# Kernel optimization log

Measured on AMD Instinct MI355X. Metric: run time of the kernel, lower is better.

The kernel has to match this reference:

```python
import jax, jax.numpy as jnp
import numpy as np

N = {"drug": 20000, "gene": 80000, "disease": 20000}
E = 800000
D = 128  # in_size = hidden_size = out_size
ETYPES = [("drug", "treats", "disease"), ("drug", "targets", "gene"),
          ("gene", "assoc", "disease"), ("disease", "rev_treats", "drug")]


def setup_inputs() -> dict:
    key = jax.random.key(0)
    ks = iter(jax.random.split(key, 64))
    inp = {}
    for nt in ["drug", "gene", "disease"]:
        inp[f"feat_{nt}"] = jax.random.normal(next(ks), (N[nt], D), jnp.float32)
    for layer in (1, 2):
        for (_, e, _) in ETYPES:
            inp[f"W{layer}_{e}"] = jax.random.normal(next(ks), (D, D), jnp.float32) / np.sqrt(D).astype(np.float32)
            inp[f"b{layer}_{e}"] = jnp.zeros((D,), jnp.float32)
    for (s, e, d) in ETYPES:
        inp[f"src_{e}"] = jax.random.randint(next(ks), (E,), 0, N[s], jnp.int32)
        inp[f"dst_{e}"] = jax.random.randint(next(ks), (E,), 0, N[d], jnp.int32)
        inp[f"neg_dst_{e}"] = jax.random.randint(next(ks), (E,), 0, N[d], jnp.int32)
    return inp


def _rgcn_layer(feats, W, b, src, dst):
    # per-etype Linear -> copy_u -> per-dst mean, summed across etypes ('sum' cross reducer)
    out = {nt: jnp.zeros((N[nt], D), jnp.float32) for nt in N}
    for (s, e, d) in ETYPES:
        Wh = feats[s] @ W[e] + b[e]                          # [N_s, D]
        msg = Wh[src[e]]                                     # [E, D] gather
        ssum = jax.ops.segment_sum(msg, dst[e], num_segments=N[d])
        cnt = jax.ops.segment_sum(jnp.ones((E,), jnp.float32), dst[e], num_segments=N[d])
        out[d] = out[d] + ssum / jnp.maximum(cnt, 1.0)[:, None]
    return out


def _dot_scores(h, src, dst):
    # DotProductPredictor: sigmoid(u . v) per edge, concatenated over etypes
    return jnp.concatenate([
        jax.nn.sigmoid(jnp.sum(h[s][src[e]] * h[d][dst[e]], axis=-1))
        for (s, e, d) in ETYPES])


def reference(feat_drug, feat_gene, feat_disease,
              W1_treats, b1_treats, W1_targets, b1_targets, W1_assoc, b1_assoc,
              W1_rev_treats, b1_rev_treats,
              W2_treats, b2_treats, W2_targets, b2_targets, W2_assoc, b2_assoc,
              W2_rev_treats, b2_rev_treats,
              src_treats, dst_treats, src_targets, dst_targets,
              src_assoc, dst_assoc, src_rev_treats, dst_rev_treats,
              neg_dst_treats, neg_dst_targets, neg_dst_assoc, neg_dst_rev_treats):
    feats = {"drug": feat_drug, "gene": feat_gene, "disease": feat_disease}
    W1 = {"treats": W1_treats, "targets": W1_targets, "assoc": W1_assoc, "rev_treats": W1_rev_treats}
    b1 = {"treats": b1_treats, "targets": b1_targets, "assoc": b1_assoc, "rev_treats": b1_rev_treats}
    W2 = {"treats": W2_treats, "targets": W2_targets, "assoc": W2_assoc, "rev_treats": W2_rev_treats}
    b2 = {"treats": b2_treats, "targets": b2_targets, "assoc": b2_assoc, "rev_treats": b2_rev_treats}
    src = {"treats": src_treats, "targets": src_targets, "assoc": src_assoc, "rev_treats": src_rev_treats}
    dst = {"treats": dst_treats, "targets": dst_targets, "assoc": dst_assoc, "rev_treats": dst_rev_treats}
    neg_dst = {"treats": neg_dst_treats, "targets": neg_dst_targets,
               "assoc": neg_dst_assoc, "rev_treats": neg_dst_rev_treats}

    h1 = _rgcn_layer(feats, W1, b1, src, dst)
    h1 = {k: jax.nn.leaky_relu(v, 0.01) for k, v in h1.items()}  # F.leaky_relu default slope
    h2 = _rgcn_layer(h1, W2, b2, src, dst)
    out_pos = _dot_scores(h2, src, dst)       # positive graph = G's own edges
    out_neg = _dot_scores(h2, src, neg_dst)   # negative graph: corrupted dst
    return jnp.concatenate([out_pos, out_neg])  # [2 * 4 * E]
```

## Files before the change

kernel.cpp:

```cpp
#include <hip/hip_runtime.h>
#include <hip/hip_bf16.h>
#include <cstddef>

#define NE 800000
#define NCNT 140000
#define NBLK 137

typedef unsigned short ushortT;

__device__ __forceinline__ float lrelu01(float x) { return x > 0.f ? x : 0.01f * x; }
__device__ __forceinline__ float blo(int v) { return __uint_as_float(((unsigned)v) << 16); }
__device__ __forceinline__ float bhi(int v) { return __uint_as_float(((unsigned)v) & 0xffff0000u); }
__device__ __forceinline__ ushortT f2b(float x) {
  unsigned u = __float_as_uint(x);
  unsigned r = (u + 0x7fffu + ((u >> 16) & 1u)) >> 16;
  return (ushortT)r;
}

__global__ __launch_bounds__(256) void count_kernel(const int* d0, const int* d1,
                                                    const int* d2, const int* d3,
                                                    int* __restrict__ cnt) {
  const int e = blockIdx.y;
  const int* dst = e == 0 ? d0 : e == 1 ? d1 : e == 2 ? d2 : d3;
  int* c = cnt + (e == 0 ? 0 : e == 1 ? 20000 : e == 2 ? 100000 : 120000);
  int stride = gridDim.x * blockDim.x;
  for (int i = blockIdx.x * blockDim.x + threadIdx.x; i < NE; i += stride)
    atomicAdd(&c[dst[i]], 1);
}

__global__ __launch_bounds__(256) void inv_kernel(const int* __restrict__ cnt,
                                                  float* __restrict__ inv, int n) {
  int i = blockIdx.x * blockDim.x + threadIdx.x;
  if (i < n) {
    int c = cnt[i];
    inv[i] = 1.0f / (float)(c > 1 ? c : 1);
  }
}

__global__ __launch_bounds__(256) void psum_kernel(const int* __restrict__ cnt,
                                                   int* __restrict__ bsum, int n) {
  __shared__ int red[4];
  const int tid = threadIdx.x;
  const int base = blockIdx.x * 1024;
  int s = 0;
#pragma unroll
  for (int k = 0; k < 4; ++k) {
    int i = base + tid + 256 * k;
    s += (i < n) ? cnt[i] : 0;
  }
#pragma unroll
  for (int off = 32; off >= 1; off >>= 1) s += __shfl_xor(s, off, 64);
  if ((tid & 63) == 0) red[tid >> 6] = s;
  __syncthreads();
  if (tid == 0) bsum[blockIdx.x] = red[0] + red[1] + red[2] + red[3];
}

__global__ __launch_bounds__(256) void bscan_kernel(const int* __restrict__ bsum,
                                                    int* __restrict__ bex,
                                                    int* __restrict__ gscan, int nb, int n) {
  __shared__ int sh[256];
  const int tid = threadIdx.x;
  sh[tid] = (tid < nb) ? bsum[tid] : 0;
  __syncthreads();
  for (int off = 1; off < 256; off <<= 1) {
    int add = (tid >= off) ? sh[tid - off] : 0;
    __syncthreads();
    sh[tid] += add;
    __syncthreads();
  }
  if (tid < nb) bex[tid] = (tid == 0) ? 0 : sh[tid - 1];
  if (tid == nb - 1) gscan[n] = sh[tid];
}

__global__ __launch_bounds__(256) void scanout_kernel(const int* __restrict__ cnt,
                                                      const int* __restrict__ bex,
                                                      int* __restrict__ gscan, int n) {
  __shared__ int part[256];
  const int tid = threadIdx.x;
  const int base = blockIdx.x * 1024 + tid * 4;
  int v0 = (base + 0 < n) ? cnt[base + 0] : 0;
  int v1 = (base + 1 < n) ? cnt[base + 1] : 0;
  int v2 = (base + 2 < n) ? cnt[base + 2] : 0;
  int v3 = (base + 3 < n) ? cnt[base + 3] : 0;
  part[tid] = v0 + v1 + v2 + v3;
  __syncthreads();
  for (int off = 1; off < 256; off <<= 1) {
    int add = (tid >= off) ? part[tid - off] : 0;
    __syncthreads();
    part[tid] += add;
    __syncthreads();
  }
  int ex = bex[blockIdx.x] + ((tid == 0) ? 0 : part[tid - 1]);
  if (base + 0 < n) gscan[base + 0] = ex;
  ex += v0;
  if (base + 1 < n) gscan[base + 1] = ex;
  ex += v1;
  if (base + 2 < n) gscan[base + 2] = ex;
  ex += v2;
  if (base + 3 < n) gscan[base + 3] = ex;
}

__global__ __launch_bounds__(256) void place_kernel(const int* s0, const int* s1,
                                                    const int* s2, const int* s3,
                                                    const int* d0, const int* d1,
                                                    const int* d2, const int* d3,
                                                    const int* __restrict__ gscan,
                                                    int* __restrict__ cursor,
                                                    int* __restrict__ csr) {
  const int e = blockIdx.y;
  const int* src = e == 0 ? s0 : e == 1 ? s1 : e == 2 ? s2 : s3;
  const int* dst = e == 0 ? d0 : e == 1 ? d1 : e == 2 ? d2 : d3;
  const int co = e == 0 ? 0 : e == 1 ? 20000 : e == 2 ? 100000 : 120000;
  const int wr = e == 0 ? 0 : e == 1 ? 20000 : e == 2 ? 40000 : 120000;
  int stride = gridDim.x * blockDim.x;
  for (int i = blockIdx.x * blockDim.x + threadIdx.x; i < NE; i += stride) {
    int d = dst[i];
    int p = gscan[co + d] + atomicAdd(&cursor[co + d], 1);
    csr[p] = src[i] + wr;
  }
}

template <bool LRELU>
__global__ __launch_bounds__(256) void gemm_kernel(const float* X0, const float* X1,
                                                   const float* X2, const float* X3,
                                                   const float* W0, const float* W1,
                                                   const float* W2, const float* W3,
                                                   const float* B0, const float* B1,
                                                   const float* B2, const float* B3,
                                                   ushortT* __restrict__ out) {
  __shared__ float Ws[128 * 128];
  __shared__ float xs[32 * 128];
  const int tid = threadIdx.x;
  const int bid = blockIdx.x;

  int lrow0, wo;
  const float *X, *W, *B;
  if (bid < 625)       { lrow0 = bid * 32;          X = X0; W = W0; B = B0; wo = 0; }
  else if (bid < 1250) { lrow0 = (bid - 625) * 32;  X = X1; W = W1; B = B1; wo = 20000; }
  else if (bid < 3750) { lrow0 = (bid - 1250) * 32; X = X2; W = W2; B = B2; wo = 40000; }
  else                 { lrow0 = (bid - 3750) * 32; X = X3; W = W3; B = B3; wo = 120000; }

  {
    const float4* Wv = (const float4*)W;
    float4* Wsv = (float4*)Ws;
#pragma unroll
    for (int i = 0; i < 16; ++i) Wsv[tid + 256 * i] = Wv[tid + 256 * i];
  }
  {
    float4* xsv = (float4*)xs;
#pragma unroll
    for (int i = 0; i < 4; ++i) {
      int f = tid + 256 * i;
      int rr = f >> 5;
      int c4 = f & 31;
      float4 v = *(const float4*)(X + (size_t)(lrow0 + rr) * 128 + c4 * 4);
      if (LRELU) {
        v.x = lrelu01(v.x); v.y = lrelu01(v.y); v.z = lrelu01(v.z); v.w = lrelu01(v.w);
      }
      xsv[f] = v;
    }
  }
  __syncthreads();

  const int c = tid & 31;
  const int r = tid >> 5;
  const float4 bv = *(const float4*)(B + c * 4);
  float acc[4][4];
#pragma unroll
  for (int ri = 0; ri < 4; ++ri) {
    acc[ri][0] = bv.x; acc[ri][1] = bv.y; acc[ri][2] = bv.z; acc[ri][3] = bv.w;
  }

#pragma unroll 8
  for (int k0 = 0; k0 < 128; k0 += 4) {
    const float4 w0 = *(const float4*)(Ws + (k0 + 0) * 128 + c * 4);
    const float4 w1 = *(const float4*)(Ws + (k0 + 1) * 128 + c * 4);
    const float4 w2 = *(const float4*)(Ws + (k0 + 2) * 128 + c * 4);
    const float4 w3 = *(const float4*)(Ws + (k0 + 3) * 128 + c * 4);
#pragma unroll
    for (int ri = 0; ri < 4; ++ri) {
      const float4 xv = *(const float4*)(xs + (r + 8 * ri) * 128 + k0);
      acc[ri][0] = fmaf(xv.x, w0.x, acc[ri][0]);
      acc[ri][0] = fmaf(xv.y, w1.x, acc[ri][0]);
      acc[ri][0] = fmaf(xv.z, w2.x, acc[ri][0]);
      acc[ri][0] = fmaf(xv.w, w3.x, acc[ri][0]);
      acc[ri][1] = fmaf(xv.x, w0.y, acc[ri][1]);
      acc[ri][1] = fmaf(xv.y, w1.y, acc[ri][1]);
      acc[ri][1] = fmaf(xv.z, w2.y, acc[ri][1]);
      acc[ri][1] = fmaf(xv.w, w3.y, acc[ri][1]);
      acc[ri][2] = fmaf(xv.x, w0.z, acc[ri][2]);
      acc[ri][2] = fmaf(xv.y, w1.z, acc[ri][2]);
      acc[ri][2] = fmaf(xv.z, w2.z, acc[ri][2]);
      acc[ri][2] = fmaf(xv.w, w3.z, acc[ri][2]);
      acc[ri][3] = fmaf(xv.x, w0.w, acc[ri][3]);
      acc[ri][3] = fmaf(xv.y, w1.w, acc[ri][3]);
      acc[ri][3] = fmaf(xv.z, w2.w, acc[ri][3]);
      acc[ri][3] = fmaf(xv.w, w3.w, acc[ri][3]);
    }
  }

#pragma unroll
  for (int ri = 0; ri < 4; ++ri) {
    int gr = wo + lrow0 + r + 8 * ri;
    ushort4 o;
    o.x = f2b(acc[ri][0]); o.y = f2b(acc[ri][1]);
    o.z = f2b(acc[ri][2]); o.w = f2b(acc[ri][3]);
    *(ushort4*)(out + (size_t)gr * 128 + c * 4) = o;
  }
}

template <bool OUT_BF16, int NSLOT>
__global__ __launch_bounds__(256) void gather_kernel(const ushortT* __restrict__ Wh,
                                                     const int* __restrict__ csr,
                                                     const int* __restrict__ gscan,
                                                     const float* __restrict__ inv,
                                                     int slot0, int slot1,
                                                     void* __restrict__ outv, int nnode) {
  const int lane = threadIdx.x & 63;
  const int q = lane >> 4;
  const int ql = lane & 15;
  int w = (blockIdx.x * blockDim.x + threadIdx.x) >> 6;
  const int nw = (gridDim.x * blockDim.x) >> 6;
  for (int d = w; d < nnode; d += nw) {
    float a0 = 0.f, a1 = 0.f, a2 = 0.f, a3 = 0.f, a4 = 0.f, a5 = 0.f, a6 = 0.f, a7 = 0.f;
#pragma unroll
    for (int k = 0; k < NSLOT; ++k) {
      const int slot = (k == 0 ? slot0 : slot1) + d;
      const int beg = gscan[slot];
      const int end = gscan[slot + 1];
      float t0 = 0.f, t1 = 0.f, t2 = 0.f, t3 = 0.f, t4 = 0.f, t5 = 0.f, t6 = 0.f, t7 = 0.f;
      for (int c0 = beg; c0 < end; c0 += 64) {
        int m = end - c0;
        if (m > 64) m = 64;
        int idx = (c0 + lane < end) ? csr[c0 + lane] : 0;
        for (int j = 0; j < m; j += 4) {
          int jj = j + q;
          int s = __shfl(idx, jj < m ? jj : 0, 64);
          if (jj < m) {
            const int4 v = *(const int4*)(Wh + (size_t)s * 128 + ql * 8);
            t0 += blo(v.x); t1 += bhi(v.x);
            t2 += blo(v.y); t3 += bhi(v.y);
            t4 += blo(v.z); t5 += bhi(v.z);
            t6 += blo(v.w); t7 += bhi(v.w);
          }
        }
      }
      const float ic = inv[slot];
      a0 = fmaf(t0, ic, a0); a1 = fmaf(t1, ic, a1);
      a2 = fmaf(t2, ic, a2); a3 = fmaf(t3, ic, a3);
      a4 = fmaf(t4, ic, a4); a5 = fmaf(t5, ic, a5);
      a6 = fmaf(t6, ic, a6); a7 = fmaf(t7, ic, a7);
    }
    a0 += __shfl_xor(a0, 16, 64); a0 += __shfl_xor(a0, 32, 64);
    a1 += __shfl_xor(a1, 16, 64); a1 += __shfl_xor(a1, 32, 64);
    a2 += __shfl_xor(a2, 16, 64); a2 += __shfl_xor(a2, 32, 64);
    a3 += __shfl_xor(a3, 16, 64); a3 += __shfl_xor(a3, 32, 64);
    a4 += __shfl_xor(a4, 16, 64); a4 += __shfl_xor(a4, 32, 64);
    a5 += __shfl_xor(a5, 16, 64); a5 += __shfl_xor(a5, 32, 64);
    a6 += __shfl_xor(a6, 16, 64); a6 += __shfl_xor(a6, 32, 64);
    a7 += __shfl_xor(a7, 16, 64); a7 += __shfl_xor(a7, 32, 64);
    if (lane < 16) {
      if (OUT_BF16) {
        ushortT* out = (ushortT*)outv;
        int4 o;
        o.x = (int)f2b(a0) | ((int)f2b(a1) << 16);
        o.y = (int)f2b(a2) | ((int)f2b(a3) << 16);
        o.z = (int)f2b(a4) | ((int)f2b(a5) << 16);
        o.w = (int)f2b(a6) | ((int)f2b(a7) << 16);
        *(int4*)(out + (size_t)d * 128 + ql * 8) = o;
      } else {
        float* out = (float*)outv;
        *(float4*)(out + (size_t)d * 128 + ql * 8) = make_float4(a0, a1, a2, a3);
        *(float4*)(out + (size_t)d * 128 + ql * 8 + 4) = make_float4(a4, a5, a6, a7);
      }
    }
  }
}

__global__ __launch_bounds__(256) void score_kernel(const ushortT* __restrict__ hs,
                                                    const ushortT* __restrict__ hd,
                                                    const int* __restrict__ src,
                                                    const int* __restrict__ dst,
                                                    const int* __restrict__ ndst,
                                                    float* __restrict__ outp,
                                                    float* __restrict__ outn) {
  const int lane = threadIdx.x & 63;
  const int q = lane >> 4;
  const int ql = lane & 15;
  int w = (blockIdx.x * blockDim.x + threadIdx.x) >> 6;
  const int nw = (gridDim.x * blockDim.x) >> 6;
  for (int base = 4 * w; base < NE; base += 4 * nw) {
    int e = base + q;
    int s = src[e], d = dst[e], n = ndst[e];
    const int4 av = *(const int4*)(hs + (size_t)s * 128 + ql * 8);
    const int4 bv = *(const int4*)(hd + (size_t)d * 128 + ql * 8);
    const int4 cv = *(const int4*)(hd + (size_t)n * 128 + ql * 8);
    float dp = blo(av.x) * blo(bv.x) + bhi(av.x) * bhi(bv.x)
             + blo(av.y) * blo(bv.y) + bhi(av.y) * bhi(bv.y)
             + blo(av.z) * blo(bv.z) + bhi(av.z) * bhi(bv.z)
             + blo(av.w) * blo(bv.w) + bhi(av.w) * bhi(bv.w);
    float dn = blo(av.x) * blo(cv.x) + bhi(av.x) * bhi(cv.x)
             + blo(av.y) * blo(cv.y) + bhi(av.y) * bhi(cv.y)
             + blo(av.z) * blo(cv.z) + bhi(av.z) * bhi(cv.z)
             + blo(av.w) * blo(cv.w) + bhi(av.w) * bhi(cv.w);
#pragma unroll
    for (int off = 1; off <= 8; off <<= 1) {
      dp += __shfl_xor(dp, off, 64);
      dn += __shfl_xor(dn, off, 64);
    }
    if (ql == 0) {
      outp[e] = 1.0f / (1.0f + expf(-dp));
      outn[e] = 1.0f / (1.0f + expf(-dn));
    }
  }
}

extern "C" void kernel_launch(void* const* d_in, const int* in_sizes, int n_in,
                              void* d_out, int out_size, void* d_ws, size_t ws_size,
                              hipStream_t stream) {
  const float* feat[3] = {(const float*)d_in[0], (const float*)d_in[1], (const float*)d_in[2]};
  const float *W1[4], *b1[4], *W2[4], *b2[4];
  for (int e = 0; e < 4; ++e) {
    W1[e] = (const float*)d_in[3 + 2 * e];
    b1[e] = (const float*)d_in[4 + 2 * e];
    W2[e] = (const float*)d_in[11 + 2 * e];
    b2[e] = (const float*)d_in[12 + 2 * e];
  }
  const int *src[4], *dst[4], *ndst[4];
  for (int e = 0; e < 4; ++e) {
    src[e] = (const int*)d_in[19 + 3 * e];
    dst[e] = (const int*)d_in[20 + 3 * e];
    ndst[e] = (const int*)d_in[21 + 3 * e];
  }

  ushortT* WhAll = (ushortT*)d_ws;
  float* h1 = (float*)(WhAll + (size_t)140000 * 128);
  ushortT* h2 = (ushortT*)(h1 + (size_t)120000 * 128);
  int* cnt = (int*)(h2 + (size_t)120000 * 128);
  float* inv = (float*)(cnt + NCNT);
  int* gscan = (int*)(inv + NCNT);
  int* cursor = gscan + NCNT + 1;
  int* bsum = cursor + NCNT;
  int* bex = bsum + 256;
  int* csr = bex + 256;

  hipMemsetAsync(cnt, 0, NCNT * 4, stream);
  hipMemsetAsync(cursor, 0, NCNT * 4, stream);

  const size_t HD = 0, HG = 20000, HS = 100000;

  count_kernel<<<dim3(512, 4), 256, 0, stream>>>(dst[0], dst[1], dst[2], dst[3], cnt);
  inv_kernel<<<(NCNT + 255) / 256, 256, 0, stream>>>(cnt, inv, NCNT);
  psum_kernel<<<NBLK, 256, 0, stream>>>(cnt, bsum, NCNT);
  bscan_kernel<<<1, 256, 0, stream>>>(bsum, bex, gscan, NBLK, NCNT);
  scanout_kernel<<<NBLK, 256, 0, stream>>>(cnt, bex, gscan, NCNT);
  place_kernel<<<dim3(512, 4), 256, 0, stream>>>(src[0], src[1], src[2], src[3],
                                                 dst[0], dst[1], dst[2], dst[3],
                                                 gscan, cursor, csr);

  gemm_kernel<false><<<4375, 256, 0, stream>>>(
      feat[0], feat[0], feat[1], feat[2],
      W1[0], W1[1], W1[2], W1[3], b1[0], b1[1], b1[2], b1[3], WhAll);
  gather_kernel<false, 1><<<2048, 256, 0, stream>>>(WhAll, csr, gscan, inv, 120000, 0,
                                                    (void*)(h1 + HD * 128), 20000);
  gather_kernel<false, 1><<<2048, 256, 0, stream>>>(WhAll, csr, gscan, inv, 20000, 0,
                                                    (void*)(h1 + HG * 128), 80000);
  gather_kernel<false, 2><<<2048, 256, 0, stream>>>(WhAll, csr, gscan, inv, 0, 100000,
                                                    (void*)(h1 + HS * 128), 20000);

  gemm_kernel<true><<<4375, 256, 0, stream>>>(
      h1 + HD * 128, h1 + HD * 128, h1 + HG * 128, h1 + HS * 128,
      W2[0], W2[1], W2[2], W2[3], b2[0], b2[1], b2[2], b2[3], WhAll);
  gather_kernel<true, 1><<<2048, 256, 0, stream>>>(WhAll, csr, gscan, inv, 120000, 0,
                                                   (void*)(h2 + HD * 128), 20000);
  gather_kernel<true, 1><<<2048, 256, 0, stream>>>(WhAll, csr, gscan, inv, 20000, 0,
                                                   (void*)(h2 + HG * 128), 80000);
  gather_kernel<true, 2><<<2048, 256, 0, stream>>>(WhAll, csr, gscan, inv, 0, 100000,
                                                   (void*)(h2 + HS * 128), 20000);

  const size_t sh[4] = {HD, HD, HG, HS};
  const size_t dh[4] = {HS, HG, HS, HD};
  float* out = (float*)d_out;
  for (int e = 0; e < 4; ++e) {
    score_kernel<<<2048, 256, 0, stream>>>(h2 + sh[e] * 128, h2 + dh[e] * 128,
                                           src[e], dst[e], ndst[e], out + (size_t)e * NE,
                                           out + (size_t)(4 + e) * NE);
  }
}
```

Baseline: 1.095 ms.

## Remap gather to quarter-wave per node, store h1 as bf16, fuse preprocessing kernels

The gather kernel now assigns one 16-lane group to each destination node instead of a full wavefront, removing the cross-group shuffle reduction and issuing four row loads per step. Layer-1 hidden features are stored as bf16, and the second GEMM reads bf16 input, which halves that traffic but adds rounding. The inverse-count computation and cursor initialisation move into the scan kernel, so one launch and one memset go away. The score kernel processes two edges per group per iteration to raise memory-level parallelism.

Result: no change. 1.092 ms (-0.2%).

```diff
diff --git a/kernel.cpp b/kernel.cpp
--- a/kernel.cpp
+++ b/kernel.cpp
@@ -26,15 +26,6 @@
   int stride = gridDim.x * blockDim.x;
   for (int i = blockIdx.x * blockDim.x + threadIdx.x; i < NE; i += stride)
     atomicAdd(&c[dst[i]], 1);
-}
-
-__global__ __launch_bounds__(256) void inv_kernel(const int* __restrict__ cnt,
-                                                  float* __restrict__ inv, int n) {
-  int i = blockIdx.x * blockDim.x + threadIdx.x;
-  if (i < n) {
-    int c = cnt[i];
-    inv[i] = 1.0f / (float)(c > 1 ? c : 1);
-  }
 }
 
 __global__ __launch_bounds__(256) void psum_kernel(const int* __restrict__ cnt,
@@ -74,7 +65,9 @@
 
 __global__ __launch_bounds__(256) void scanout_kernel(const int* __restrict__ cnt,
                                                       const int* __restrict__ bex,
-                                                      int* __restrict__ gscan, int n) {
+                                                      int* __restrict__ gscan,
+                                                      int* __restrict__ cursor,
+                                                      float* __restrict__ inv, int n) {
   __shared__ int part[256];
   const int tid = threadIdx.x;
   const int base = blockIdx.x * 1024 + tid * 4;
@@ -91,20 +84,19 @@
     __syncthreads();
   }
   int ex = bex[blockIdx.x] + ((tid == 0) ? 0 : part[tid - 1]);
-  if (base + 0 < n) gscan[base + 0] = ex;
+  if (base + 0 < n) { gscan[base+0] = ex; cursor[base+0] = ex; inv[base+0] = 1.0f/(float)(v0>1?v0:1); }
   ex += v0;
-  if (base + 1 < n) gscan[base + 1] = ex;
+  if (base + 1 < n) { gscan[base+1] = ex; cursor[base+1] = ex; inv[base+1] = 1.0f/(float)(v1>1?v1:1); }
   ex += v1;
-  if (base + 2 < n) gscan[base + 2] = ex;
+  if (base + 2 < n) { gscan[base+2] = ex; cursor[base+2] = ex; inv[base+2] = 1.0f/(float)(v2>1?v2:1); }
   ex += v2;
-  if (base + 3 < n) gscan[base + 3] = ex;
+  if (base + 3 < n) { gscan[base+3] = ex; cursor[base+3] = ex; inv[base+3] = 1.0f/(float)(v3>1?v3:1); }
 }
 
 __global__ __launch_bounds__(256) void place_kernel(const int* s0, const int* s1,
                                                     const int* s2, const int* s3,
                                                     const int* d0, const int* d1,
                                                     const int* d2, const int* d3,
-                                                    const int* __restrict__ gscan,
                                                     int* __restrict__ cursor,
                                                     int* __restrict__ csr) {
   const int e = blockIdx.y;
@@ -114,15 +106,14 @@
   const int wr = e == 0 ? 0 : e == 1 ? 20000 : e == 2 ? 40000 : 120000;
   int stride = gridDim.x * blockDim.x;
   for (int i = blockIdx.x * blockDim.x + threadIdx.x; i < NE; i += stride) {
-    int d = dst[i];
-    int p = gscan[co + d] + atomicAdd(&cursor[co + d], 1);
+    int p = atomicAdd(&cursor[co + dst[i]], 1);
     csr[p] = src[i] + wr;
   }
 }
 
-template <bool LRELU>
-__global__ __launch_bounds__(256) void gemm_kernel(const float* X0, const float* X1,
-                                                   const float* X2, const float* X3,
+template <bool LRELU, bool XBF16>
+__global__ __launch_bounds__(256) void gemm_kernel(const void* X0v, const void* X1v,
+                                                   const void* X2v, const void* X3v,
                                                    const float* W0, const float* W1,
                                                    const float* W2, const float* W3,
                                                    const float* B0, const float* B1,
@@ -134,11 +125,12 @@
   const int bid = blockIdx.x;
 
   int lrow0, wo;
-  const float *X, *W, *B;
-  if (bid < 625)       { lrow0 = bid * 32;          X = X0; W = W0; B = B0; wo = 0; }
-  else if (bid < 1250) { lrow0 = (bid - 625) * 32;  X = X1; W = W1; B = B1; wo = 20000; }
-  else if (bid < 3750) { lrow0 = (bid - 1250) * 32; X = X2; W = W2; B = B2; wo = 40000; }
-  else                 { lrow0 = (bid - 3750) * 32; X = X3; W = W3; B = B3; wo = 120000; }
+  const void* Xv;
+  const float *W, *B;
+  if (bid < 625)       { lrow0 = bid * 32;          Xv = X0v; W = W0; B = B0; wo = 0; }
+  else if (bid < 1250) { lrow0 = (bid - 625) * 32;  Xv = X1v; W = W1; B = B1; wo = 20000; }
+  else if (bid < 3750) { lrow0 = (bid - 1250) * 32; Xv = X2v; W = W2; B = B2; wo = 40000; }
+  else                 { lrow0 = (bid - 3750) * 32; Xv = X3v; W = W3; B = B3; wo = 120000; }
 
   {
     const float4* Wv = (const float4*)W;
@@ -146,7 +138,26 @@
 #pragma unroll
     for (int i = 0; i < 16; ++i) Wsv[tid + 256 * i] = Wv[tid + 256 * i];
   }
-  {
+  if (XBF16) {
+    const ushortT* X = (const ushortT*)Xv;
+#pragma unroll
+    for (int i = 0; i < 2; ++i) {
+      int f = tid + 256 * i;
+      int rr = f >> 4;
+      int c8 = f & 15;
+      int4 v = *(const int4*)(X + (size_t)(lrow0 + rr) * 128 + c8 * 8);
+      float x0 = blo(v.x), x1 = bhi(v.x), x2 = blo(v.y), x3 = bhi(v.y);
+      float x4 = blo(v.z), x5 = bhi(v.z), x6 = blo(v.w), x7 = bhi(v.w);
+      if (LRELU) {
+        x0 = lrelu01(x0); x1 = lrelu01(x1); x2 = lrelu01(x2); x3 = lrelu01(x3);
+        x4 = lrelu01(x4); x5 = lrelu01(x5); x6 = lrelu01(x6); x7 = lrelu01(x7);
+      }
+      float* p = xs + rr * 128 + c8 * 8;
+      *(float4*)(p) = make_float4(x0, x1, x2, x3);
+      *(float4*)(p + 4) = make_float4(x4, x5, x6, x7);
+    }
+  } else {
+    const float* X = (const float*)Xv;
     float4* xsv = (float4*)xs;
 #pragma unroll
     for (int i = 0; i < 4; ++i) {
@@ -209,72 +220,63 @@
   }
 }
 
-template <bool OUT_BF16, int NSLOT>
+template <int NSLOT>
 __global__ __launch_bounds__(256) void gather_kernel(const ushortT* __restrict__ Wh,
                                                      const int* __restrict__ csr,
                                                      const int* __restrict__ gscan,
                                                      const float* __restrict__ inv,
                                                      int slot0, int slot1,
-                                                     void* __restrict__ outv, int nnode) {
+                                                     ushortT* __restrict__ out, int nnode) {
   const int lane = threadIdx.x & 63;
-  const int q = lane >> 4;
   const int ql = lane & 15;
-  int w = (blockIdx.x * blockDim.x + threadIdx.x) >> 6;
-  const int nw = (gridDim.x * blockDim.x) >> 6;
-  for (int d = w; d < nnode; d += nw) {
-    float a0 = 0.f, a1 = 0.f, a2 = 0.f, a3 = 0.f, a4 = 0.f, a5 = 0.f, a6 = 0.f, a7 = 0.f;
-#pragma unroll
-    for (int k = 0; k < NSLOT; ++k) {
-      const int slot = (k == 0 ? slot0 : slot1) + d;
-      const int beg = gscan[slot];
-      const int end = gscan[slot + 1];
-      float t0 = 0.f, t1 = 0.f, t2 = 0.f, t3 = 0.f, t4 = 0.f, t5 = 0.f, t6 = 0.f, t7 = 0.f;
-      for (int c0 = beg; c0 < end; c0 += 64) {
-        int m = end - c0;
-        if (m > 64) m = 64;
-        int idx = (c0 + lane < end) ? csr[c0 + lane] : 0;
-        for (int j = 0; j < m; j += 4) {
-          int jj = j + q;
-          int s = __shfl(idx, jj < m ? jj : 0, 64);
-          if (jj < m) {
-            const int4 v = *(const int4*)(Wh + (size_t)s * 128 + ql * 8);
-            t0 += blo(v.x); t1 += bhi(v.x);
-            t2 += blo(v.y); t3 += bhi(v.y);
-            t4 += blo(v.z); t5 += bhi(v.z);
-            t6 += blo(v.w); t7 += bhi(v.w);
-          }
-        }
+  const int qbase = lane & 48;
+  const int d = (blockIdx.x * blockDim.x + threadIdx.x) >> 4;
+  if (d >= nnode) return;
+  float a0 = 0.f, a1 = 0.f, a2 = 0.f, a3 = 0.f, a4 = 0.f, a5 = 0.f, a6 = 0.f, a7 = 0.f;
+#pragma unroll
+  for (int k = 0; k < NSLOT; ++k) {
+    const int slot = (k == 0 ? slot0 : slot1) + d;
+    const int beg = gscan[slot];
+    const int end = gscan[slot + 1];
+    float t0 = 0.f, t1 = 0.f, t2 = 0.f, t3 = 0.f, t4 = 0.f, t5 = 0.f, t6 = 0.f, t7 = 0.f;
+    for (int c0 = beg; c0 < end; c0 += 16) {
+      int m = end - c0;
+      if (m > 16) m = 16;
+      int idx = (c0 + ql < end) ? csr[c0 + ql] : 0;
+      for (int j = 0; j < m; j += 4) {
+        int s0 = __shfl(idx, qbase + j, 64);
+        int s1 = __shfl(idx, qbase + j + 1, 64);
+        int s2 = __shfl(idx, qbase + j + 2, 64);
+        int s3 = __shfl(idx, qbase + j + 3, 64);
+        const int4 v0 = *(const int4*)(Wh + (size_t)s0 * 128 + ql * 8);
+        const int4 v1 = *(const int4*)(Wh + (size_t)s1 * 128 + ql * 8);
+        const int4 v2 = *(const int4*)(Wh + (size_t)s2 * 128 + ql * 8);
+        const int4 v3 = *(const int4*)(Wh + (size_t)s3 * 128 + ql * 8);
+        const float w1 = (j + 1 < m) ? 1.f : 0.f;
+        const float w2 = (j + 2 < m) ? 1.f : 0.f;
+        const float w3 = (j + 3 < m) ? 1.f : 0.f;
+        t0 += blo(v0.x); t0 = fmaf(w1, blo(v1.x), t0); t0 = fmaf(w2, blo(v2.x), t0); t0 = fmaf(w3, blo(v3.x), t0);
+        t1 += bhi(v0.x); t1 = fmaf(w1, bhi(v1.x), t1); t1 = fmaf(w2, bhi(v2.x), t1); t1 = fmaf(w3, bhi(v3.x), t1);
+        t2 += blo(v0.y); t2 = fmaf(w1, blo(v1.y), t2); t2 = fmaf(w2, blo(v2.y), t2); t2 = fmaf(w3, blo(v3.y), t2);
+        t3 += bhi(v0.y); t3 = fmaf(w1, bhi(v1.y), t3); t3 = fmaf(w2, bhi(v2.y), t3); t3 = fmaf(w3, bhi(v3.y), t3);
+        t4 += blo(v0.z); t4 = fmaf(w1, blo(v1.z), t4); t4 = fmaf(w2, blo(v2.z), t4); t4 = fmaf(w3, blo(v3.z), t4);
+        t5 += bhi(v0.z); t5 = fmaf(w1, bhi(v1.z), t5); t5 = fmaf(w2, bhi(v2.z), t5); t5 = fmaf(w3, bhi(v3.z), t5);
+        t6 += blo(v0.w); t6 = fmaf(w1, blo(v1.w), t6); t6 = fmaf(w2, blo(v2.w), t6); t6 = fmaf(w3, blo(v3.w), t6);
+        t7 += bhi(v0.w); t7 = fmaf(w1, bhi(v1.w), t7); t7 = fmaf(w2, bhi(v2.w), t7); t7 = fmaf(w3, bhi(v3.w), t7);
       }
-      const float ic = inv[slot];
-      a0 = fmaf(t0, ic, a0); a1 = fmaf(t1, ic, a1);
-      a2 = fmaf(t2, ic, a2); a3 = fmaf(t3, ic, a3);
-      a4 = fmaf(t4, ic, a4); a5 = fmaf(t5, ic, a5);
-      a6 = fmaf(t6, ic, a6); a7 = fmaf(t7, ic, a7);
-    }
-    a0 += __shfl_xor(a0, 16, 64); a0 += __shfl_xor(a0, 32, 64);
-    a1 += __shfl_xor(a1, 16, 64); a1 += __shfl_xor(a1, 32, 64);
-    a2 += __shfl_xor(a2, 16, 64); a2 += __shfl_xor(a2, 32, 64);
-    a3 += __shfl_xor(a3, 16, 64); a3 += __shfl_xor(a3, 32, 64);
-    a4 += __shfl_xor(a4, 16, 64); a4 += __shfl_xor(a4, 32, 64);
-    a5 += __shfl_xor(a5, 16, 64); a5 += __shfl_xor(a5, 32, 64);
-    a6 += __shfl_xor(a6, 16, 64); a6 += __shfl_xor(a6, 32, 64);
-    a7 += __shfl_xor(a7, 16, 64); a7 += __shfl_xor(a7, 32, 64);
-    if (lane < 16) {
-      if (OUT_BF16) {
-        ushortT* out = (ushortT*)outv;
-        int4 o;
-        o.x = (int)f2b(a0) | ((int)f2b(a1) << 16);
-        o.y = (int)f2b(a2) | ((int)f2b(a3) << 16);
-        o.z = (int)f2b(a4) | ((int)f2b(a5) << 16);
-        o.w = (int)f2b(a6) | ((int)f2b(a7) << 16);
-        *(int4*)(out + (size_t)d * 128 + ql * 8) = o;
-      } else {
-        float* out = (float*)outv;
-        *(float4*)(out + (size_t)d * 128 + ql * 8) = make_float4(a0, a1, a2, a3);
-        *(float4*)(out + (size_t)d * 128 + ql * 8 + 4) = make_float4(a4, a5, a6, a7);
-      }
-    }
-  }
+    }
+    const float ic = inv[slot];
+    a0 = fmaf(t0, ic, a0); a1 = fmaf(t1, ic, a1);
+    a2 = fmaf(t2, ic, a2); a3 = fmaf(t3, ic, a3);
+    a4 = fmaf(t4, ic, a4); a5 = fmaf(t5, ic, a5);
+    a6 = fmaf(t6, ic, a6); a7 = fmaf(t7, ic, a7);
+  }
+  int4 o;
+  o.x = (int)f2b(a0) | ((int)f2b(a1) << 16);
+  o.y = (int)f2b(a2) | ((int)f2b(a3) << 16);
+  o.z = (int)f2b(a4) | ((int)f2b(a5) << 16);
+  o.w = (int)f2b(a6) | ((int)f2b(a7) << 16);
+  *(int4*)(out + (size_t)d * 128 + ql * 8) = o;
 }
 
 __global__ __launch_bounds__(256) void score_kernel(const ushortT* __restrict__ hs,
@@ -289,28 +291,45 @@
   const int ql = lane & 15;
   int w = (blockIdx.x * blockDim.x + threadIdx.x) >> 6;
   const int nw = (gridDim.x * blockDim.x) >> 6;
-  for (int base = 4 * w; base < NE; base += 4 * nw) {
-    int e = base + q;
-    int s = src[e], d = dst[e], n = ndst[e];
-    const int4 av = *(const int4*)(hs + (size_t)s * 128 + ql * 8);
-    const int4 bv = *(const int4*)(hd + (size_t)d * 128 + ql * 8);
-    const int4 cv = *(const int4*)(hd + (size_t)n * 128 + ql * 8);
-    float dp = blo(av.x) * blo(bv.x) + bhi(av.x) * bhi(bv.x)
-             + blo(av.y) * blo(bv.y) + bhi(av.y) * bhi(bv.y)
-             + blo(av.z) * blo(bv.z) + bhi(av.z) * bhi(bv.z)
-             + blo(av.w) * blo(bv.w) + bhi(av.w) * bhi(bv.w);
-    float dn = blo(av.x) * blo(cv.x) + bhi(av.x) * bhi(cv.x)
-             + blo(av.y) * blo(cv.y) + bhi(av.y) * bhi(cv.y)
-             + blo(av.z) * blo(cv.z) + bhi(av.z) * bhi(cv.z)
-             + blo(av.w) * blo(cv.w) + bhi(av.w) * bhi(cv.w);
+  for (int base = 8 * w; base < NE; base += 8 * nw) {
+    int e1 = base + q;
+    int e2 = base + 4 + q;
+    int s1 = src[e1], d1 = dst[e1], n1 = ndst[e1];
+    int s2 = src[e2], d2 = dst[e2], n2 = ndst[e2];
+    const int4 av1 = *(const int4*)(hs + (size_t)s1 * 128 + ql * 8);
+    const int4 bv1 = *(const int4*)(hd + (size_t)d1 * 128 + ql * 8);
+    const int4 cv1 = *(const int4*)(hd + (size_t)n1 * 128 + ql * 8);
+    const int4 av2 = *(const int4*)(hs + (size_t)s2 * 128 + ql * 8);
+    const int4 bv2 = *(const int4*)(hd + (size_t)d2 * 128 + ql * 8);
+    const int4 cv2 = *(const int4*)(hd + (size_t)n2 * 128 + ql * 8);
+    float dp1 = blo(av1.x) * blo(bv1.x) + bhi(av1.x) * bhi(bv1.x)
+              + blo(av1.y) * blo(bv1.y) + bhi(av1.y) * bhi(bv1.y)
+              + blo(av1.z) * blo(bv1.z) + bhi(av1.z) * bhi(bv1.z)
+              + blo(av1.w) * blo(bv1.w) + bhi(av1.w) * bhi(bv1.w);
+    float dn1 = blo(av1.x) * blo(cv1.x) + bhi(av1.x) * bhi(cv1.x)
+              + blo(av1.y) * blo(cv1.y) + bhi(av1.y) * bhi(cv1.y)
+              + blo(av1.z) * blo(cv1.z) + bhi(av1.z) * bhi(cv1.z)
+              + blo(av1.w) * blo(cv1.w) + bhi(av1.w) * bhi(cv1.w);
+    float dp2 = blo(av2.x) * blo(bv2.x) + bhi(av2.x) * bhi(bv2.x)
+              + blo(av2.y) * blo(bv2.y) + bhi(av2.y) * bhi(bv2.y)
+              + blo(av2.z) * blo(bv2.z) + bhi(av2.z) * bhi(bv2.z)
+              + blo(av2.w) * blo(bv2.w) + bhi(av2.w) * bhi(bv2.w);
+    float dn2 = blo(av2.x) * blo(cv2.x) + bhi(av2.x) * bhi(cv2.x)
+              + blo(av2.y) * blo(cv2.y) + bhi(av2.y) * bhi(cv2.y)
+              + blo(av2.z) * blo(cv2.z) + bhi(av2.z) * bhi(cv2.z)
+              + blo(av2.w) * blo(cv2.w) + bhi(av2.w) * bhi(cv2.w);
 #pragma unroll
     for (int off = 1; off <= 8; off <<= 1) {
-      dp += __shfl_xor(dp, off, 64);
-      dn += __shfl_xor(dn, off, 64);
+      dp1 += __shfl_xor(dp1, off, 64);
+      dn1 += __shfl_xor(dn1, off, 64);
+      dp2 += __shfl_xor(dp2, off, 64);
+      dn2 += __shfl_xor(dn2, off, 64);
     }
     if (ql == 0) {
-      outp[e] = 1.0f / (1.0f + expf(-dp));
-      outn[e] = 1.0f / (1.0f + expf(-dn));
+      outp[e1] = 1.0f / (1.0f + expf(-dp1));
+      outn[e1] = 1.0f / (1.0f + expf(-dn1));
+      outp[e2] = 1.0f / (1.0f + expf(-dp2));
+      outn[e2] = 1.0f / (1.0f + expf(-dn2));
     }
   }
 }
@@ -334,8 +353,8 @@
   }
 
   ushortT* WhAll = (ushortT*)d_ws;
-  float* h1 = (float*)(WhAll + (size_t)140000 * 128);
-  ushortT* h2 = (ushortT*)(h1 + (size_t)120000 * 128);
+  ushortT* h1 = WhAll + (size_t)140000 * 128;
+  ushortT* h2 = h1 + (size_t)120000 * 128;
   int* cnt = (int*)(h2 + (size_t)120000 * 128);
   float* inv = (float*)(cnt + NCNT);
   int* gscan = (int*)(inv + NCNT);
@@ -345,38 +364,30 @@
   int* csr = bex + 256;
 
   hipMemsetAsync(cnt, 0, NCNT * 4, stream);
-  hipMemsetAsync(cursor, 0, NCNT * 4, stream);
 
   const size_t HD = 0, HG = 20000, HS = 100000;
 
   count_kernel<<<dim3(512, 4), 256, 0, stream>>>(dst[0], dst[1], dst[2], dst[3], cnt);
-  inv_kernel<<<(NCNT + 255) / 256, 256, 0, stream>>>(cnt, inv, NCNT);
   psum_kernel<<<NBLK, 256, 0, stream>>>(cnt, bsum, NCNT);
   bscan_kernel<<<1, 256, 0, stream>>>(bsum, bex, gscan, NBLK, NCNT);
-  scanout_kernel<<<NBLK, 256, 0, stream>>>(cnt, bex, gscan, NCNT);
+  scanout_kernel<<<NBLK, 256, 0, stream>>>(cnt, bex, gscan, cursor, inv, NCNT);
   place_kernel<<<dim3(512, 4), 256, 0, stream>>>(src[0], src[1], src[2], src[3],
                                                  dst[0], dst[1], dst[2], dst[3],
-                                                 gscan, cursor, csr);
-
-  gemm_kernel<false><<<4375, 256, 0, stream>>>(
+                                                 cursor, csr);
+
+  gemm_kernel<false, false><<<4375, 256, 0, stream>>>(
       feat[0], feat[0], feat[1], feat[2],
       W1[0], W1[1], W1[2], W1[3], b1[0], b1[1], b1[2], b1[3], WhAll);
-  gather_kernel<false, 1><<<2048, 256, 0, stream>>>(WhAll, csr, gscan, inv, 120000, 0,
-                                                    (void*)(h1 + HD * 128), 20000);
-  gather_kernel<false, 1><<<2048, 256, 0, stream>>>(WhAll, csr, gscan, inv, 20000, 0,
-                                                    (void*)(h1 + HG * 128), 80000);
-  gather_kernel<false, 2><<<2048, 256, 0, stream>>>(WhAll, csr, gscan, inv, 0, 100000,
-                                                    (void*)(h1 + HS * 128), 20000);
-
-  gemm_kernel<true><<<4375, 256, 0, stream>>>(
+  gather_kernel<1><<<1250, 256, 0, stream>>>(WhAll, csr, gscan, inv, 120000, 0, h1 + HD * 128, 20000);
+  gather_kernel<1><<<5000, 256, 0, stream>>>(WhAll, csr, gscan, inv, 20000, 0, h1 + HG * 128, 80000);
+  gather_kernel<2><<<1250, 256, 0, stream>>>(WhAll, csr, gscan, inv, 0, 100000, h1 + HS * 128, 20000);
+
+  gemm_kernel<true, true><<<4375, 256, 0, stream>>>(
       h1 + HD * 128, h1 + HD * 128, h1 + HG * 128, h1 + HS * 128,
       W2[0], W2[1], W2[2], W2[3], b2[0], b2[1], b2[2], b2[3], WhAll);
-  gather_kernel<true, 1><<<2048, 256, 0, stream>>>(WhAll, csr, gscan, inv, 120000, 0,
-                                                   (void*)(h2 + HD * 128), 20000);
-  gather_kernel<true, 1><<<2048, 256, 0, stream>>>(WhAll, csr, gscan, inv, 20000, 0,
-                                                   (void*)(h2 + HG * 128), 80000);
-  gather_kernel<true, 2><<<2048, 256, 0, stream>>>(WhAll, csr, gscan, inv, 0, 100000,
-                                                   (void*)(h2 + HS * 128), 20000);
+  gather_kernel<1><<<1250, 256, 0, stream>>>(WhAll, csr, gscan, inv, 120000, 0, h2 + HD * 128, 20000);
+  gather_kernel<1><<<5000, 256, 0, stream>>>(WhAll, csr, gscan, inv, 20000, 0, h2 + HG * 128, 80000);
+  gather_kernel<2><<<1250, 256, 0, stream>>>(WhAll, csr, gscan, inv, 0, 100000, h2 + HS * 128, 20000);
 
   const size_t sh[4] = {HD, HD, HG, HS};
   const size_t dh[4] = {HS, HG, HS, HD};
```
